# Kernel optimization log

Measured on AMD Instinct MI355X. Metric: run time of the kernel, lower is better.

The kernel has to match this reference:

```python
import jax, jax.numpy as jnp
import numpy as np

EMBED_DIM = 1024
NUM_HEADS = 16
HEAD_DIM = EMBED_DIM // NUM_HEADS


def setup_inputs() -> dict:
    key = jax.random.key(0)
    ks = jax.random.split(key, 11)
    D = EMBED_DIM
    s = 1.0 / np.sqrt(D)
    x = jax.random.normal(ks[0], (2, 2048, D), dtype=jnp.float32)
    # nn.Linear weights are [out, in]; we store transposed [in, out] for x @ W.
    Wq = jax.random.uniform(ks[1], (D, D), jnp.float32, -s, s)
    bq = jax.random.uniform(ks[2], (D,), jnp.float32, -s, s)
    Wk = jax.random.uniform(ks[3], (D, D), jnp.float32, -s, s)
    bk = jax.random.uniform(ks[4], (D,), jnp.float32, -s, s)
    Wv = jax.random.uniform(ks[5], (D, D), jnp.float32, -s, s)
    bv = jax.random.uniform(ks[6], (D,), jnp.float32, -s, s)
    Wo = jax.random.uniform(ks[7], (D, D), jnp.float32, -s, s)
    bo = jax.random.uniform(ks[8], (D,), jnp.float32, -s, s)
    ln_g = jnp.ones((D,), jnp.float32)
    ln_b = jnp.zeros((D,), jnp.float32)
    return {"x": x, "Wq": Wq, "bq": bq, "Wk": Wk, "bk": bk,
            "Wv": Wv, "bv": bv, "Wo": Wo, "bo": bo,
            "ln_g": ln_g, "ln_b": ln_b}


def _layernorm(x, g, b, eps=1e-5):
    mu = jnp.mean(x, axis=-1, keepdims=True)
    var = jnp.mean(jnp.square(x - mu), axis=-1, keepdims=True)
    return (x - mu) * jax.lax.rsqrt(var + eps) * g + b


def reference(x, Wq, bq, Wk, bk, Wv, bv, Wo, bo, ln_g, ln_b):
    B, T, D = x.shape
    H, Hd = NUM_HEADS, HEAD_DIM
    # [B,T,D] -> [B,H,T,Hd]
    def split_heads(y):
        return y.reshape(B, T, H, Hd).transpose(0, 2, 1, 3)
    q = split_heads(x @ Wq + bq)
    k = split_heads(x @ Wk + bk)
    v = split_heads(x @ Wv + bv)
    scores = jnp.einsum('bhqd,bhkd->bhqk', q, k) / jnp.sqrt(jnp.float32(Hd))
    attn = jax.nn.softmax(scores, axis=-1)
    o = jnp.einsum('bhqk,bhkd->bhqd', attn, v)
    o = o.transpose(0, 2, 1, 3).reshape(B, T, D)
    out = o @ Wo + bo
    return _layernorm(out + x, ln_g, ln_b)
```

## Files before the change

kernel.cpp:

```cpp
#include <hip/hip_runtime.h>
#include <hip/hip_bf16.h>
#include <stdint.h>
#include <math.h>

#define B_ 2
#define T_ 2048
#define D_ 1024
#define H_ 16
#define HD_ 64
#define M_ 4096

using bf16 = __hip_bfloat16;
using short8 = __attribute__((ext_vector_type(8))) short;
using f32x4 = __attribute__((ext_vector_type(4))) float;

__device__ __forceinline__ void async16(const void* g, void* l) {
  __builtin_amdgcn_global_load_lds((const __attribute__((address_space(1))) void*)g,
                                   (__attribute__((address_space(3))) void*)l, 16, 0, 0);
}

__global__ __launch_bounds__(256) void cast_x(const float* __restrict__ x, bf16* __restrict__ xb) {
  const int i = (blockIdx.x * 256 + threadIdx.x) * 8;
  float4 a = *(const float4*)(x + i);
  float4 b = *(const float4*)(x + i + 4);
  bf16 o[8] = { __float2bfloat16(a.x), __float2bfloat16(a.y), __float2bfloat16(a.z), __float2bfloat16(a.w),
                __float2bfloat16(b.x), __float2bfloat16(b.y), __float2bfloat16(b.z), __float2bfloat16(b.w) };
  *(uint4*)(xb + i) = *(const uint4*)o;
}

__global__ __launch_bounds__(256) void transpose4(const float* __restrict__ wq, const float* __restrict__ wk,
                                                  const float* __restrict__ wv, const float* __restrict__ wo,
                                                  bf16* __restrict__ wt) {
  __shared__ float tile[32][33];
  const int which = blockIdx.z;
  const float* src = which==0?wq:which==1?wk:which==2?wv:wo;
  bf16* dst = wt + ((size_t)which << 20);
  const int tx = threadIdx.x, ty = threadIdx.y;
  const int row0 = blockIdx.y*32;
  const int col  = blockIdx.x*32 + tx;
  #pragma unroll
  for (int j=ty; j<32; j+=8) tile[j][tx] = src[(size_t)(row0+j)*D_ + col];
  __syncthreads();
  const int ocol  = row0 + tx;
  const int orow0 = blockIdx.x*32;
  #pragma unroll
  for (int j=ty; j<32; j+=8) dst[(size_t)(orow0+j)*D_ + ocol] = __float2bfloat16(tile[tx][j]);
}

__global__ __launch_bounds__(256,1) void qkv_gemm(const bf16* __restrict__ X, const bf16* __restrict__ Wt,
                                                  const float* __restrict__ bq, const float* __restrict__ bk,
                                                  const float* __restrict__ bv,
                                                  bf16* __restrict__ Qb, bf16* __restrict__ Kb, bf16* __restrict__ Vb) {
  __shared__ bf16 As[128*32];
  __shared__ bf16 Bs[128*32];
  const int tid = threadIdx.x;
  const int lane = tid & 63, wave = tid >> 6;
  const int quad = lane >> 4, l16 = lane & 15;
  const int wm = (wave >> 1) * 64, wn = (wave & 1) * 64;
  const int m0  = blockIdx.x * 128;
  const int nt0 = blockIdx.y * 128;
  const int which = nt0 >> 10;
  const int n0 = nt0 & 1023;
  const bf16* W = Wt + ((size_t)which << 20);
  const float* bias = which==0 ? bq : (which==1 ? bk : bv);
  const bool vmode = (which == 2);
  const float oscale = (which==0) ? 0.125f * 1.44269504088896340736f : 1.0f;

  f32x4 acc[4][4];
  #pragma unroll
  for (int i=0;i<4;i++)
    #pragma unroll
    for (int j=0;j<4;j++) acc[i][j] = (f32x4){0.f,0.f,0.f,0.f};

  for (int k0 = 0; k0 < 1024; k0 += 32) {
    __syncthreads();
    #pragma unroll
    for (int it=0; it<2; ++it) {
      int id = tid + it*256;
      int row = id >> 2, seg = id & 3;
      async16(X + (size_t)(m0+row)*1024 + k0 + seg*8, (char*)As + id*16);
      async16(W + (size_t)(n0+row)*1024 + k0 + seg*8, (char*)Bs + id*16);
    }
    __syncthreads();
    const bf16* Asrc = vmode ? Bs : As;
    const bf16* Bsrc = vmode ? As : Bs;
    short8 af[4], bfv[4];
    #pragma unroll
    for (int i=0;i<4;i++) af[i]  = *(const short8*)(Asrc + (wm + i*16 + l16)*32 + quad*8);
    #pragma unroll
    for (int j=0;j<4;j++) bfv[j] = *(const short8*)(Bsrc + (wn + j*16 + l16)*32 + quad*8);
    #pragma unroll
    for (int i=0;i<4;i++)
      #pragma unroll
      for (int j=0;j<4;j++)
        acc[i][j] = __builtin_amdgcn_mfma_f32_16x16x32_bf16(af[i], bfv[j], acc[i][j], 0, 0, 0);
  }

  if (!vmode) {
    bf16* out = (which==0) ? Qb : Kb;
    #pragma unroll
    for (int i=0;i<4;i++) {
      #pragma unroll
      for (int j=0;j<4;j++) {
        const int n = n0 + wn + j*16 + l16;
        const float bvv = bias[n];
        const int h = n >> 6, hd = n & 63;
        #pragma unroll
        for (int r=0;r<4;r++) {
          const int m = m0 + wm + i*16 + quad*4 + r;
          const int b = m >> 11, t = m & 2047;
          out[(((size_t)b*H_ + h)*T_ + t)*HD_ + hd] = __float2bfloat16((acc[i][j][r] + bvv) * oscale);
        }
      }
    }
  } else {
    #pragma unroll
    for (int i=0;i<4;i++) {
      #pragma unroll
      for (int r=0;r<4;r++) {
        const int n = n0 + wm + i*16 + quad*4 + r;
        const float bvv = bias[n];
        const int h = n >> 6, hd = n & 63;
        #pragma unroll
        for (int j=0;j<4;j++) {
          const int m = m0 + wn + j*16 + l16;
          const int b = m >> 11, t = m & 2047;
          Vb[(((size_t)b*H_ + h)*HD_ + hd)*T_ + t] = __float2bfloat16(acc[i][j][r] + bvv);
        }
      }
    }
  }
}

__device__ __forceinline__ void stage64x64(const bf16* __restrict__ g, size_t gstride, bf16* lds,
                                           int wave, int lane) {
  const int lr = lane >> 3;
  const int c  = (lane & 7) ^ lr;
  #pragma unroll
  for (int it = 0; it < 2; ++it) {
    const int group = wave * 2 + it;
    async16(g + (size_t)(group*8 + lr)*gstride + c*8, lds + group*512 + lane*8);
  }
}

__device__ __forceinline__ short8 read_swz(const bf16* lds, int row, int chunk) {
  return *(const short8*)(lds + row*64 + ((chunk ^ (row & 7)) << 3));
}

#define PSTR 68

__global__ __launch_bounds__(256,2) void attn_kernel(const bf16* __restrict__ Qg, const bf16* __restrict__ Kg,
                                                     const bf16* __restrict__ Vg, bf16* __restrict__ Og) {
  __shared__ bf16 Qs[128*64];
  __shared__ bf16 Kd[2][64*64];
  __shared__ bf16 Vd[2][64*64];
  __shared__ bf16 Ps[4][16*PSTR];

  const int tid = threadIdx.x;
  const int lane = tid & 63, wave = tid >> 6;
  const int quad = lane >> 4, l16 = lane & 15;
  const int bh = blockIdx.y;
  const int q0 = blockIdx.x * 128;

  const bf16* Qp = Qg + (size_t)bh*T_*HD_;
  const bf16* Kp = Kg + (size_t)bh*T_*HD_;
  const bf16* Vp = Vg + (size_t)bh*HD_*T_;

  stage64x64(Qp + (size_t)q0*HD_,      HD_, Qs,       wave, lane);
  stage64x64(Qp + (size_t)(q0+64)*HD_, HD_, Qs+64*64, wave, lane);
  stage64x64(Kp, HD_, Kd[0], wave, lane);
  stage64x64(Vp, T_,  Vd[0], wave, lane);
  __syncthreads();

  short8 qf[2][2];
  #pragma unroll
  for (int s=0; s<2; ++s)
    #pragma unroll
    for (int ks=0; ks<2; ++ks)
      qf[s][ks] = read_swz(Qs + s*64*64, wave*16 + l16, ks*4 + quad);

  f32x4 o_acc[2][4];
  float l_part[2] = {0.f, 0.f};
  #pragma unroll
  for (int s=0;s<2;s++)
    #pragma unroll
    for (int jv=0;jv<4;jv++) o_acc[s][jv] = (f32x4){0.f,0.f,0.f,0.f};

  bf16* Pw = &Ps[wave][0];
  const int NT = T_/64;

  for (int kt=0; kt<NT; ++kt) {
    const int cur = kt & 1;
    if (kt+1 < NT) {
      stage64x64(Kp + (size_t)(kt+1)*64*HD_, HD_, Kd[1-cur], wave, lane);
      stage64x64(Vp + (size_t)(kt+1)*64,     T_,  Vd[1-cur], wave, lane);
    }
    const bf16* Ks  = Kd[cur];
    const bf16* Vts = Vd[cur];

    short8 kf[2][4], vf[2][4];
    #pragma unroll
    for (int ks=0; ks<2; ++ks)
      #pragma unroll
      for (int j=0; j<4; ++j) {
        kf[ks][j] = read_swz(Ks,  j*16 + l16, ks*4 + quad);
        vf[ks][j] = read_swz(Vts, j*16 + l16, ks*4 + quad);
      }

    f32x4 s0[4];
    #pragma unroll
    for (int jb=0;jb<4;jb++) s0[jb] = (f32x4){0.f,0.f,0.f,0.f};
    #pragma unroll
    for (int ks=0; ks<2; ++ks)
      #pragma unroll
      for (int jb=0;jb<4;jb++)
        s0[jb] = __builtin_amdgcn_mfma_f32_16x16x32_bf16(kf[ks][jb], qf[0][ks], s0[jb], 0, 0, 0);

    #pragma unroll
    for (int jb=0;jb<4;jb++) {
      bf16 pk[4];
      #pragma unroll
      for (int r=0;r<4;r++) {
        float pv = __builtin_amdgcn_exp2f(s0[jb][r]);
        l_part[0] += pv;
        pk[r] = __float2bfloat16(pv);
      }
      *(uint2*)(&Pw[l16*PSTR + jb*16 + quad*4]) = *(const uint2*)pk;
    }

    f32x4 s1[4];
    #pragma unroll
    for (int jb=0;jb<4;jb++) s1[jb] = (f32x4){0.f,0.f,0.f,0.f};
    #pragma unroll
    for (int ks=0; ks<2; ++ks)
      #pragma unroll
      for (int jb=0;jb<4;jb++)
        s1[jb] = __builtin_amdgcn_mfma_f32_16x16x32_bf16(kf[ks][jb], qf[1][ks], s1[jb], 0, 0, 0);

    #pragma unroll
    for (int ks=0; ks<2; ++ks) {
      short8 pf = *(const short8*)(&Pw[l16*PSTR + ks*32 + quad*8]);
      #pragma unroll
      for (int jv=0;jv<4;jv++)
        o_acc[0][jv] = __builtin_amdgcn_mfma_f32_16x16x32_bf16(pf, vf[ks][jv], o_acc[0][jv], 0, 0, 0);
    }

    #pragma unroll
    for (int jb=0;jb<4;jb++) {
      bf16 pk[4];
      #pragma unroll
      for (int r=0;r<4;r++) {
        float pv = __builtin_amdgcn_exp2f(s1[jb][r]);
        l_part[1] += pv;
        pk[r] = __float2bfloat16(pv);
      }
      *(uint2*)(&Pw[l16*PSTR + jb*16 + quad*4]) = *(const uint2*)pk;
    }

    #pragma unroll
    for (int ks=0; ks<2; ++ks) {
      short8 pf = *(const short8*)(&Pw[l16*PSTR + ks*32 + quad*8]);
      #pragma unroll
      for (int jv=0;jv<4;jv++)
        o_acc[1][jv] = __builtin_amdgcn_mfma_f32_16x16x32_bf16(pf, vf[ks][jv], o_acc[1][jv], 0, 0, 0);
    }

    __syncthreads();
  }

  float linv[2][4];
  #pragma unroll
  for (int s=0;s<2;s++) {
    float l = l_part[s];
    l += __shfl_xor(l, 16);
    l += __shfl_xor(l, 32);
    const float inv = 1.0f / l;
    #pragma unroll
    for (int r=0;r<4;r++) linv[s][r] = __shfl(inv, quad*4 + r);
  }

  const int b = bh >> 4, h = bh & 15;
  #pragma unroll
  for (int s=0;s<2;s++)
    #pragma unroll
    for (int jv=0;jv<4;jv++)
      #pragma unroll
      for (int r=0;r<4;r++) {
        const int row = q0 + s*64 + wave*16 + quad*4 + r;
        const float ov = o_acc[s][jv][r] * linv[s][r];
        Og[((size_t)b*T_ + row)*D_ + h*HD_ + jv*16 + l16] = __float2bfloat16(ov);
      }
}

__global__ __launch_bounds__(256,1) void proj_gemm(const bf16* __restrict__ A, const bf16* __restrict__ Wt,
                                                   const float* __restrict__ bo, const float* __restrict__ Xres,
                                                   float* __restrict__ tmp) {
  __shared__ bf16 As[128*32];
  __shared__ bf16 Bs[128*32];
  const int tid = threadIdx.x;
  const int lane = tid & 63, wave = tid >> 6;
  const int quad = lane >> 4, l16 = lane & 15;
  const int wm = (wave >> 1) * 64, wn = (wave & 1) * 64;
  const int m0 = blockIdx.x * 128;
  const int n0 = blockIdx.y * 128;

  f32x4 acc[4][4];
  #pragma unroll
  for (int i=0;i<4;i++)
    #pragma unroll
    for (int j=0;j<4;j++) acc[i][j] = (f32x4){0.f,0.f,0.f,0.f};

  for (int k0 = 0; k0 < 1024; k0 += 32) {
    __syncthreads();
    #pragma unroll
    for (int it=0; it<2; ++it) {
      int id = tid + it*256;
      int row = id >> 2, seg = id & 3;
      async16(A  + (size_t)(m0+row)*1024 + k0 + seg*8, (char*)As + id*16);
      async16(Wt + (size_t)(n0+row)*1024 + k0 + seg*8, (char*)Bs + id*16);
    }
    __syncthreads();
    short8 af[4], bfv[4];
    #pragma unroll
    for (int i=0;i<4;i++) af[i]  = *(const short8*)(As + (wm + i*16 + l16)*32 + quad*8);
    #pragma unroll
    for (int j=0;j<4;j++) bfv[j] = *(const short8*)(Bs + (wn + j*16 + l16)*32 + quad*8);
    #pragma unroll
    for (int i=0;i<4;i++)
      #pragma unroll
      for (int j=0;j<4;j++)
        acc[i][j] = __builtin_amdgcn_mfma_f32_16x16x32_bf16(af[i], bfv[j], acc[i][j], 0, 0, 0);
  }

  #pragma unroll
  for (int i=0;i<4;i++) {
    #pragma unroll
    for (int j=0;j<4;j++) {
      const int n = n0 + wn + j*16 + l16;
      const float bvv = bo[n];
      #pragma unroll
      for (int r=0;r<4;r++) {
        const int m = m0 + wm + i*16 + quad*4 + r;
        tmp[(size_t)m*1024 + n] = acc[i][j][r] + bvv + Xres[(size_t)m*1024 + n];
      }
    }
  }
}

__global__ __launch_bounds__(256) void ln_kernel(const float* __restrict__ tmp, const float* __restrict__ g,
                                                 const float* __restrict__ b, float* __restrict__ out) {
  const int row = blockIdx.x;
  const int tid = threadIdx.x;
  const float* p = tmp + (size_t)row*D_;
  float4 v = *(const float4*)(p + tid*4);
  float s  = v.x + v.y + v.z + v.w;
  float sq = v.x*v.x + v.y*v.y + v.z*v.z + v.w*v.w;
  #pragma unroll
  for (int off=32; off>0; off>>=1) { s += __shfl_down(s, off); sq += __shfl_down(sq, off); }
  __shared__ float red[8];
  __shared__ float stats[2];
  const int wave = tid >> 6, lane = tid & 63;
  if (lane == 0) { red[wave] = s; red[4+wave] = sq; }
  __syncthreads();
  if (tid == 0) {
    float S = red[0]+red[1]+red[2]+red[3];
    float Q = red[4]+red[5]+red[6]+red[7];
    float mu = S * (1.0f/D_);
    float var = Q * (1.0f/D_) - mu*mu;
    stats[0] = mu;
    stats[1] = rsqrtf(var + 1e-5f);
  }
  __syncthreads();
  const float mu = stats[0], rstd = stats[1];
  const float vals[4] = {v.x, v.y, v.z, v.w};
  float4 o;
  float* op = (float*)&o;
  #pragma unroll
  for (int c=0;c<4;c++) op[c] = (vals[c]-mu)*rstd*g[tid*4+c] + b[tid*4+c];
  *(float4*)(out + (size_t)row*D_ + tid*4) = o;
}

extern "C" void kernel_launch(void* const* d_in, const int* in_sizes, int n_in,
                              void* d_out, int out_size, void* d_ws, size_t ws_size,
                              hipStream_t stream) {
  (void)in_sizes; (void)n_in; (void)out_size; (void)ws_size;
  const float* x  = (const float*)d_in[0];
  const float* Wq = (const float*)d_in[1];
  const float* bq = (const float*)d_in[2];
  const float* Wk = (const float*)d_in[3];
  const float* bk = (const float*)d_in[4];
  const float* Wv = (const float*)d_in[5];
  const float* bv = (const float*)d_in[6];
  const float* Wo = (const float*)d_in[7];
  const float* bo = (const float*)d_in[8];
  const float* lg = (const float*)d_in[9];
  const float* lb = (const float*)d_in[10];
  float* out = (float*)d_out;

  char* ws = (char*)d_ws;
  bf16* wt  = (bf16*)ws;  ws += (size_t)4*1024*1024*sizeof(bf16);
  bf16* Xb  = (bf16*)ws;  ws += (size_t)M_*D_*sizeof(bf16);
  bf16* Vb  = (bf16*)ws;  ws += (size_t)M_*D_*sizeof(bf16);
  bf16* Ob  = (bf16*)ws;  ws += (size_t)M_*D_*sizeof(bf16);
  bf16* Qb  = (bf16*)ws;  ws += (size_t)M_*D_*sizeof(bf16);
  bf16* Kb  = (bf16*)ws;  ws += (size_t)M_*D_*sizeof(bf16);
  float* tmp = (float*)Qb;

  cast_x<<<M_*D_/(256*8), 256, 0, stream>>>(x, Xb);
  transpose4<<<dim3(32,32,4), dim3(32,8), 0, stream>>>(Wq, Wk, Wv, Wo, wt);
  qkv_gemm<<<dim3(32,24), 256, 0, stream>>>(Xb, wt, bq, bk, bv, Qb, Kb, Vb);
  attn_kernel<<<dim3(T_/128, B_*H_), 256, 0, stream>>>(Qb, Kb, Vb, Ob);
  proj_gemm<<<dim3(32,8), 256, 0, stream>>>(Ob, wt + (size_t)3*1024*1024, bo, x, tmp);
  ln_kernel<<<M_, 256, 0, stream>>>(tmp, lg, lb, out);
}
```

Before: 238.7 us.

## Split attention KV tiles across waves and merge cast/transpose prep kernels

The attention kernel now splits its waves two ways: each wave handles 64 query rows (four 16-row groups) and one half of each 64-key tile, instead of 16×2 query rows over the full key tile. This cuts per-wave K/V LDS fragment reads and lets one P tile feed the PV MFMA with a single k-step. Partial O accumulators and row sums are then reduced across wave pairs through LDS at the end. The x cast and the weight transposes are also fused into one launch (z=4 slice casts x), removing one kernel launch. The trade-off is more accumulator registers (o_acc[4][4]) and extra LDS and sync for the final reduction.

```diff
diff --git a/kernel.cpp b/kernel.cpp
--- a/kernel.cpp
+++ b/kernel.cpp
@@ -19,32 +19,37 @@
                                    (__attribute__((address_space(3))) void*)l, 16, 0, 0);
 }
 
-__global__ __launch_bounds__(256) void cast_x(const float* __restrict__ x, bf16* __restrict__ xb) {
-  const int i = (blockIdx.x * 256 + threadIdx.x) * 8;
-  float4 a = *(const float4*)(x + i);
-  float4 b = *(const float4*)(x + i + 4);
-  bf16 o[8] = { __float2bfloat16(a.x), __float2bfloat16(a.y), __float2bfloat16(a.z), __float2bfloat16(a.w),
-                __float2bfloat16(b.x), __float2bfloat16(b.y), __float2bfloat16(b.z), __float2bfloat16(b.w) };
-  *(uint4*)(xb + i) = *(const uint4*)o;
-}
-
-__global__ __launch_bounds__(256) void transpose4(const float* __restrict__ wq, const float* __restrict__ wk,
-                                                  const float* __restrict__ wv, const float* __restrict__ wo,
-                                                  bf16* __restrict__ wt) {
-  __shared__ float tile[32][33];
-  const int which = blockIdx.z;
-  const float* src = which==0?wq:which==1?wk:which==2?wv:wo;
-  bf16* dst = wt + ((size_t)which << 20);
+__global__ __launch_bounds__(256) void prep_kernel(const float* __restrict__ wq, const float* __restrict__ wk,
+                                                   const float* __restrict__ wv, const float* __restrict__ wo,
+                                                   const float* __restrict__ x,
+                                                   bf16* __restrict__ wt, bf16* __restrict__ xb) {
+  const int z = blockIdx.z;
   const int tx = threadIdx.x, ty = threadIdx.y;
-  const int row0 = blockIdx.y*32;
-  const int col  = blockIdx.x*32 + tx;
-  #pragma unroll
-  for (int j=ty; j<32; j+=8) tile[j][tx] = src[(size_t)(row0+j)*D_ + col];
-  __syncthreads();
-  const int ocol  = row0 + tx;
-  const int orow0 = blockIdx.x*32;
-  #pragma unroll
-  for (int j=ty; j<32; j+=8) dst[(size_t)(orow0+j)*D_ + ocol] = __float2bfloat16(tile[tx][j]);
+  if (z < 4) {
+    __shared__ float tile[32][33];
+    const float* src = z==0?wq:z==1?wk:z==2?wv:wo;
+    bf16* dst = wt + ((size_t)z << 20);
+    const int row0 = blockIdx.y*32;
+    const int col  = blockIdx.x*32 + tx;
+    #pragma unroll
+    for (int j=ty; j<32; j+=8) tile[j][tx] = src[(size_t)(row0+j)*D_ + col];
+    __syncthreads();
+    const int ocol  = row0 + tx;
+    const int orow0 = blockIdx.x*32;
+    #pragma unroll
+    for (int j=ty; j<32; j+=8) dst[(size_t)(orow0+j)*D_ + ocol] = __float2bfloat16(tile[tx][j]);
+  } else {
+    const int tid = ty*32 + tx;
+    const size_t base = ((size_t)(blockIdx.y*32 + blockIdx.x))*4096 + (size_t)tid*16;
+    #pragma unroll
+    for (int h=0; h<2; ++h) {
+      float4 a = *(const float4*)(x + base + h*8);
+      float4 b = *(const float4*)(x + base + h*8 + 4);
+      bf16 o[8] = { __float2bfloat16(a.x), __float2bfloat16(a.y), __float2bfloat16(a.z), __float2bfloat16(a.w),
+                    __float2bfloat16(b.x), __float2bfloat16(b.y), __float2bfloat16(b.z), __float2bfloat16(b.w) };
+      *(uint4*)(xb + base + h*8) = *(const uint4*)o;
+    }
+  }
 }
 
 __global__ __launch_bounds__(256,1) void qkv_gemm(const bf16* __restrict__ X, const bf16* __restrict__ Wt,
@@ -147,18 +152,20 @@
   return *(const short8*)(lds + row*64 + ((chunk ^ (row & 7)) << 3));
 }
 
-#define PSTR 68
+#define PSTR 36
 
 __global__ __launch_bounds__(256,2) void attn_kernel(const bf16* __restrict__ Qg, const bf16* __restrict__ Kg,
                                                      const bf16* __restrict__ Vg, bf16* __restrict__ Og) {
   __shared__ bf16 Qs[128*64];
   __shared__ bf16 Kd[2][64*64];
   __shared__ bf16 Vd[2][64*64];
-  __shared__ bf16 Ps[4][16*PSTR];
+  __shared__ bf16 Ps[4][4][16*PSTR];
+  __shared__ float Lred[2][2][4][16];
 
   const int tid = threadIdx.x;
   const int lane = tid & 63, wave = tid >> 6;
   const int quad = lane >> 4, l16 = lane & 15;
+  const int qhalf = wave & 1, khalf = wave >> 1;
   const int bh = blockIdx.y;
   const int q0 = blockIdx.x * 128;
 
@@ -172,21 +179,21 @@
   stage64x64(Vp, T_,  Vd[0], wave, lane);
   __syncthreads();
 
-  short8 qf[2][2];
-  #pragma unroll
-  for (int s=0; s<2; ++s)
+  short8 qf[4][2];
+  #pragma unroll
+  for (int s=0; s<4; ++s)
     #pragma unroll
     for (int ks=0; ks<2; ++ks)
-      qf[s][ks] = read_swz(Qs + s*64*64, wave*16 + l16, ks*4 + quad);
-
-  f32x4 o_acc[2][4];
-  float l_part[2] = {0.f, 0.f};
-  #pragma unroll
-  for (int s=0;s<2;s++)
+      qf[s][ks] = read_swz(Qs, qhalf*64 + s*16 + l16, ks*4 + quad);
+
+  f32x4 o_acc[4][4];
+  float l_part[4] = {0.f, 0.f, 0.f, 0.f};
+  #pragma unroll
+  for (int s=0;s<4;s++)
     #pragma unroll
     for (int jv=0;jv<4;jv++) o_acc[s][jv] = (f32x4){0.f,0.f,0.f,0.f};
 
-  bf16* Pw = &Ps[wave][0];
+  const int krow = khalf * 32;
   const int NT = T_/64;
 
   for (int kt=0; kt<NT; ++kt) {
@@ -198,98 +205,106 @@
     const bf16* Ks  = Kd[cur];
     const bf16* Vts = Vd[cur];
 
-    short8 kf[2][4], vf[2][4];
-    #pragma unroll
-    for (int ks=0; ks<2; ++ks)
-      #pragma unroll
-      for (int j=0; j<4; ++j) {
-        kf[ks][j] = read_swz(Ks,  j*16 + l16, ks*4 + quad);
-        vf[ks][j] = read_swz(Vts, j*16 + l16, ks*4 + quad);
+    short8 kf[2][2];
+    #pragma unroll
+    for (int jb=0; jb<2; ++jb)
+      #pragma unroll
+      for (int ks=0; ks<2; ++ks)
+        kf[jb][ks] = read_swz(Ks, krow + jb*16 + l16, ks*4 + quad);
+    short8 vf[4];
+    #pragma unroll
+    for (int jv=0; jv<4; ++jv)
+      vf[jv] = read_swz(Vts, jv*16 + l16, khalf*4 + quad);
+
+    #pragma unroll
+    for (int s=0; s<4; ++s) {
+      f32x4 sc[2];
+      sc[0] = (f32x4){0.f,0.f,0.f,0.f};
+      sc[1] = (f32x4){0.f,0.f,0.f,0.f};
+      #pragma unroll
+      for (int ks=0; ks<2; ++ks)
+        #pragma unroll
+        for (int jb=0; jb<2; ++jb)
+          sc[jb] = __builtin_amdgcn_mfma_f32_16x16x32_bf16(kf[jb][ks], qf[s][ks], sc[jb], 0, 0, 0);
+      bf16* Pw = &Ps[wave][s][0];
+      #pragma unroll
+      for (int jb=0; jb<2; ++jb) {
+        bf16 pk[4];
+        #pragma unroll
+        for (int r=0; r<4; ++r) {
+          float pv = __builtin_amdgcn_exp2f(sc[jb][r]);
+          l_part[s] += pv;
+          pk[r] = __float2bfloat16(pv);
+        }
+        *(uint2*)(&Pw[l16*PSTR + jb*16 + quad*4]) = *(const uint2*)pk;
       }
-
-    f32x4 s0[4];
-    #pragma unroll
-    for (int jb=0;jb<4;jb++) s0[jb] = (f32x4){0.f,0.f,0.f,0.f};
-    #pragma unroll
-    for (int ks=0; ks<2; ++ks)
-      #pragma unroll
-      for (int jb=0;jb<4;jb++)
-        s0[jb] = __builtin_amdgcn_mfma_f32_16x16x32_bf16(kf[ks][jb], qf[0][ks], s0[jb], 0, 0, 0);
-
-    #pragma unroll
-    for (int jb=0;jb<4;jb++) {
-      bf16 pk[4];
-      #pragma unroll
-      for (int r=0;r<4;r++) {
-        float pv = __builtin_amdgcn_exp2f(s0[jb][r]);
-        l_part[0] += pv;
-        pk[r] = __float2bfloat16(pv);
-      }
-      *(uint2*)(&Pw[l16*PSTR + jb*16 + quad*4]) = *(const uint2*)pk;
-    }
-
-    f32x4 s1[4];
-    #pragma unroll
-    for (int jb=0;jb<4;jb++) s1[jb] = (f32x4){0.f,0.f,0.f,0.f};
-    #pragma unroll
-    for (int ks=0; ks<2; ++ks)
-      #pragma unroll
-      for (int jb=0;jb<4;jb++)
-        s1[jb] = __builtin_amdgcn_mfma_f32_16x16x32_bf16(kf[ks][jb], qf[1][ks], s1[jb], 0, 0, 0);
-
-    #pragma unroll
-    for (int ks=0; ks<2; ++ks) {
-      short8 pf = *(const short8*)(&Pw[l16*PSTR + ks*32 + quad*8]);
-      #pragma unroll
-      for (int jv=0;jv<4;jv++)
-        o_acc[0][jv] = __builtin_amdgcn_mfma_f32_16x16x32_bf16(pf, vf[ks][jv], o_acc[0][jv], 0, 0, 0);
-    }
-
-    #pragma unroll
-    for (int jb=0;jb<4;jb++) {
-      bf16 pk[4];
-      #pragma unroll
-      for (int r=0;r<4;r++) {
-        float pv = __builtin_amdgcn_exp2f(s1[jb][r]);
-        l_part[1] += pv;
-        pk[r] = __float2bfloat16(pv);
-      }
-      *(uint2*)(&Pw[l16*PSTR + jb*16 + quad*4]) = *(const uint2*)pk;
-    }
-
-    #pragma unroll
-    for (int ks=0; ks<2; ++ks) {
-      short8 pf = *(const short8*)(&Pw[l16*PSTR + ks*32 + quad*8]);
-      #pragma unroll
-      for (int jv=0;jv<4;jv++)
-        o_acc[1][jv] = __builtin_amdgcn_mfma_f32_16x16x32_bf16(pf, vf[ks][jv], o_acc[1][jv], 0, 0, 0);
-    }
-
-    __syncthreads();
-  }
-
-  float linv[2][4];
-  #pragma unroll
-  for (int s=0;s<2;s++) {
+    }
+
+    #pragma unroll
+    for (int s=0; s<4; ++s) {
+      short8 pf = *(const short8*)(&Ps[wave][s][l16*PSTR + quad*8]);
+      #pragma unroll
+      for (int jv=0; jv<4; ++jv)
+        o_acc[s][jv] = __builtin_amdgcn_mfma_f32_16x16x32_bf16(pf, vf[jv], o_acc[s][jv], 0, 0, 0);
+    }
+
+    __syncthreads();
+  }
+
+  #pragma unroll
+  for (int s=0; s<4; ++s) {
     float l = l_part[s];
     l += __shfl_xor(l, 16);
     l += __shfl_xor(l, 32);
-    const float inv = 1.0f / l;
-    #pragma unroll
-    for (int r=0;r<4;r++) linv[s][r] = __shfl(inv, quad*4 + r);
-  }
-
-  const int b = bh >> 4, h = bh & 15;
-  #pragma unroll
-  for (int s=0;s<2;s++)
-    #pragma unroll
-    for (int jv=0;jv<4;jv++)
-      #pragma unroll
-      for (int r=0;r<4;r++) {
-        const int row = q0 + s*64 + wave*16 + quad*4 + r;
-        const float ov = o_acc[s][jv][r] * linv[s][r];
-        Og[((size_t)b*T_ + row)*D_ + h*HD_ + jv*16 + l16] = __float2bfloat16(ov);
-      }
+    l_part[s] = l;
+  }
+  if (lane < 16) {
+    #pragma unroll
+    for (int s=0; s<4; ++s) Lred[qhalf][khalf][s][lane] = l_part[s];
+  }
+  __syncthreads();
+  float linv[4][4];
+  #pragma unroll
+  for (int s=0; s<4; ++s)
+    #pragma unroll
+    for (int r=0; r<4; ++r)
+      linv[s][r] = 1.0f / (Lred[qhalf][0][s][quad*4+r] + Lred[qhalf][1][s][quad*4+r]);
+
+  f32x4* xb = (f32x4*)Qs;
+  #pragma unroll
+  for (int round=0; round<2; ++round) {
+    const int sB = round*2;
+    if (khalf == 1) {
+      #pragma unroll
+      for (int s2=0; s2<2; ++s2)
+        #pragma unroll
+        for (int jv=0; jv<4; ++jv)
+          xb[qhalf*512 + s2*256 + jv*64 + lane] = o_acc[sB+s2][jv];
+    }
+    __syncthreads();
+    if (khalf == 0) {
+      #pragma unroll
+      for (int s2=0; s2<2; ++s2)
+        #pragma unroll
+        for (int jv=0; jv<4; ++jv)
+          o_acc[sB+s2][jv] += xb[qhalf*512 + s2*256 + jv*64 + lane];
+    }
+    __syncthreads();
+  }
+
+  if (khalf == 0) {
+    const int b = bh >> 4, h = bh & 15;
+    #pragma unroll
+    for (int s=0; s<4; ++s)
+      #pragma unroll
+      for (int jv=0; jv<4; ++jv)
+        #pragma unroll
+        for (int r=0; r<4; ++r) {
+          const int row = q0 + qhalf*64 + s*16 + quad*4 + r;
+          const float ov = o_acc[s][jv][r] * linv[s][r];
+          Og[((size_t)b*T_ + row)*D_ + h*HD_ + jv*16 + l16] = __float2bfloat16(ov);
+        }
+  }
 }
 
 __global__ __launch_bounds__(256,1) void proj_gemm(const bf16* __restrict__ A, const bf16* __restrict__ Wt,
@@ -406,8 +421,7 @@
   bf16* Kb  = (bf16*)ws;  ws += (size_t)M_*D_*sizeof(bf16);
   float* tmp = (float*)Qb;
 
-  cast_x<<<M_*D_/(256*8), 256, 0, stream>>>(x, Xb);
-  transpose4<<<dim3(32,32,4), dim3(32,8), 0, stream>>>(Wq, Wk, Wv, Wo, wt);
+  prep_kernel<<<dim3(32,32,5), dim3(32,8), 0, stream>>>(Wq, Wk, Wv, Wo, x, wt, Xb);
   qkv_gemm<<<dim3(32,24), 256, 0, stream>>>(Xb, wt, bq, bk, bv, Qb, Kb, Vb);
   attn_kernel<<<dim3(T_/128, B_*H_), 256, 0, stream>>>(Qb, Kb, Vb, Ob);
   proj_gemm<<<dim3(32,8), 256, 0, stream>>>(Ob, wt + (size_t)3*1024*1024, bo, x, tmp);
```

Measured after the change: 218.8 us. 8.3% less time.
